# Kernel tuning notes

Measured on AMD Instinct MI355X. Metric: run time of the kernel, lower is better.

Reference implementation:

```python
import jax, jax.numpy as jnp
import numpy as np

N, D, H = 262144, 512, 128


def _mlp(x, W1, b1, W2, b2):
    # Linear -> ReLU -> Linear
    return jax.nn.relu(x @ W1 + b1) @ W2 + b2


def setup_inputs() -> dict:
    key = jax.random.key(0)
    ks = jax.random.split(key, 8)
    features = jax.random.normal(ks[0], (N, D), dtype=jnp.float32)
    # last column is the routing flag: 0 -> transform expert, nonzero -> actor expert
    flags = jax.random.randint(ks[1], (N,), 0, 2).astype(jnp.float32)
    features = features.at[:, -1].set(flags)
    s = 0.02
    return {
        "features": features,
        "Wt1": jax.random.normal(ks[2], (D, H), dtype=jnp.float32) * s,
        "bt1": jnp.zeros((H,), dtype=jnp.float32),
        "Wt2": jax.random.normal(ks[3], (H, H), dtype=jnp.float32) * s,
        "bt2": jnp.zeros((H,), dtype=jnp.float32),
        "Wa1": jax.random.normal(ks[4], (D, H), dtype=jnp.float32) * s,
        "ba1": jnp.zeros((H,), dtype=jnp.float32),
        "Wa2": jax.random.normal(ks[5], (H, H), dtype=jnp.float32) * s,
        "ba2": jnp.zeros((H,), dtype=jnp.float32),
        "Wv1": jax.random.normal(ks[6], (D, H), dtype=jnp.float32) * s,
        "bv1": jnp.zeros((H,), dtype=jnp.float32),
        "Wv2": jax.random.normal(ks[7], (H, H), dtype=jnp.float32) * s,
        "bv2": jnp.zeros((H,), dtype=jnp.float32),
    }


def reference(features, Wt1, bt1, Wt2, bt2, Wa1, ba1, Wa2, ba2, Wv1, bv1, Wv2, bv2):
    # forward_actor: per-row dispatch on flag = features[:, -1]
    # flag == 0 -> policy_transform_net, else -> policy_actor_net.
    # Equivalent vectorized form: compute both experts, select per row.
    flag_is_zero = (features[:, -1] == 0)[:, None]  # [N, 1]
    trans_out = _mlp(features, Wt1, bt1, Wt2, bt2)   # [N, H]
    actor_out = _mlp(features, Wa1, ba1, Wa2, ba2)   # [N, H]
    latent_pi = jnp.where(flag_is_zero, trans_out, actor_out)
    # forward_critic: Linear-ReLU-Linear-ReLU
    latent_vf = jax.nn.relu(_mlp(features, Wv1, bv1, Wv2, bv2))
    return latent_pi, latent_vf
```

## Files before the change

kernel.cpp:

```cpp
#include <hip/hip_runtime.h>

#define NTOK 262144L

typedef __attribute__((ext_vector_type(4))) float f32x4;
typedef __attribute__((ext_vector_type(8))) short bf16x8;

static __device__ __forceinline__ unsigned short f2bf(float f) {
  unsigned int u = __builtin_bit_cast(unsigned int, f);
  u += 0x7fffu + ((u >> 16) & 1u);
  return (unsigned short)(u >> 16);
}

__global__ void pack_w(const float* __restrict__ Wt1, const float* __restrict__ Wa1,
                       const float* __restrict__ Wv1, const float* __restrict__ Wt2,
                       const float* __restrict__ Wa2, const float* __restrict__ Wv2,
                       unsigned short* __restrict__ pk) {
  int idx = blockIdx.x * 256 + threadIdx.x;
  if (idx >= 245760) return;
  float v;
  if (idx < 196608) {
    int j = idx & 7, l = (idx >> 3) & 63, ct = (idx >> 9) & 7, kt = (idx >> 12) & 15, e = idx >> 16;
    const float* W = (e == 0) ? Wt1 : (e == 1) ? Wa1 : Wv1;
    v = W[(kt * 32 + ((l >> 4) * 8) + j) * 128 + ct * 16 + (l & 15)];
  } else {
    int i2 = idx - 196608;
    int j = i2 & 7, l = (i2 >> 3) & 63, ct = (i2 >> 9) & 7, kt = (i2 >> 12) & 3, e = i2 >> 14;
    const float* W = (e == 0) ? Wt2 : (e == 1) ? Wa2 : Wv2;
    v = W[(kt * 32 + ((l >> 4) * 8) + j) * 128 + ct * 16 + (l & 15)];
  }
  pk[idx] = f2bf(v);
}


__global__ __launch_bounds__(256, 4) void mlp3(
    const float* __restrict__ X, const unsigned short* __restrict__ pk,
    const float* __restrict__ bt1, const float* __restrict__ bt2,
    const float* __restrict__ ba1, const float* __restrict__ ba2,
    const float* __restrict__ bv1, const float* __restrict__ bv2,
    float* __restrict__ out) {
  __shared__ unsigned short Xs[2 * 32 * 128];
  __shared__ unsigned short H0[32 * 128];
  __shared__ unsigned short H1[32 * 128];
  const int t = threadIdx.x;
  const long brow = (long)blockIdx.x * 32;
  const int lane = t & 63;
  const int w = t >> 6;
  const int l15 = lane & 15;
  const int g = lane >> 4;

  const float4* __restrict__ Xv = (const float4*)(X + brow * 512);

  f32x4 at[2][2], aa[2][2], av[2][2];
  #pragma unroll
  for (int c = 0; c < 2; ++c) {
    float b0 = bt1[(2 * w + c) * 16 + l15];
    float b1v = ba1[(2 * w + c) * 16 + l15];
    float b2v = bv1[(2 * w + c) * 16 + l15];
    #pragma unroll
    for (int rt = 0; rt < 2; ++rt) {
      at[rt][c] = (f32x4){b0, b0, b0, b0};
      aa[rt][c] = (f32x4){b1v, b1v, b1v, b1v};
      av[rt][c] = (f32x4){b2v, b2v, b2v, b2v};
    }
  }

  {
    float4 ld[4];
    #pragma unroll
    for (int i = 0; i < 4; ++i) {
      int f = t + 256 * i;
      ld[i] = Xv[(f >> 5) * 128 + (f & 31)];
    }
    #pragma unroll
    for (int i = 0; i < 4; ++i) {
      int f = t + 256 * i;
      int row = f >> 5, c4 = f & 31;
      unsigned long long p = (unsigned long long)f2bf(ld[i].x)
                           | ((unsigned long long)f2bf(ld[i].y) << 16)
                           | ((unsigned long long)f2bf(ld[i].z) << 32)
                           | ((unsigned long long)f2bf(ld[i].w) << 48);
      int addr = (row * 256 + c4 * 8) ^ ((row & 7) << 4);
      *(unsigned long long*)((char*)Xs + addr) = p;
    }
  }
  __syncthreads();

  unsigned fmask = 0;

  #pragma unroll
  for (int kc = 0; kc < 4; ++kc) {
    float4 nx[4];
    if (kc < 3) {
      #pragma unroll
      for (int i = 0; i < 4; ++i) {
        int f = t + 256 * i;
        nx[i] = Xv[(f >> 5) * 128 + (kc + 1) * 32 + (f & 31)];
      }
    }
    const char* xb = (const char*)Xs + (kc & 1) * 8192;
    #pragma unroll
    for (int ktl = 0; ktl < 4; ++ktl) {
      int kt = kc * 4 + ktl;
      int wo0 = ((kt * 8 + 2 * w) << 9) + (lane << 3);
      bf16x8 wt0 = *(const bf16x8*)(pk + wo0);
      bf16x8 wt1v = *(const bf16x8*)(pk + wo0 + 512);
      bf16x8 wa0 = *(const bf16x8*)(pk + 65536 + wo0);
      bf16x8 wa1v = *(const bf16x8*)(pk + 65536 + wo0 + 512);
      bf16x8 wv0 = *(const bf16x8*)(pk + 131072 + wo0);
      bf16x8 wv1v = *(const bf16x8*)(pk + 131072 + wo0 + 512);
      #pragma unroll
      for (int rt = 0; rt < 2; ++rt) {
        int row = rt * 16 + l15;
        bf16x8 a = *(const bf16x8*)(xb + ((row * 256 + ktl * 64 + g * 16) ^ ((row & 7) << 4)));
        at[rt][0] = __builtin_amdgcn_mfma_f32_16x16x32_bf16(a, wt0, at[rt][0], 0, 0, 0);
        at[rt][1] = __builtin_amdgcn_mfma_f32_16x16x32_bf16(a, wt1v, at[rt][1], 0, 0, 0);
        aa[rt][0] = __builtin_amdgcn_mfma_f32_16x16x32_bf16(a, wa0, aa[rt][0], 0, 0, 0);
        aa[rt][1] = __builtin_amdgcn_mfma_f32_16x16x32_bf16(a, wa1v, aa[rt][1], 0, 0, 0);
        av[rt][0] = __builtin_amdgcn_mfma_f32_16x16x32_bf16(a, wv0, av[rt][0], 0, 0, 0);
        av[rt][1] = __builtin_amdgcn_mfma_f32_16x16x32_bf16(a, wv1v, av[rt][1], 0, 0, 0);
      }
    }
    if (kc == 3) {
      #pragma unroll
      for (int rt = 0; rt < 2; ++rt)
        #pragma unroll
        for (int r = 0; r < 4; ++r) {
          int row = rt * 16 + 4 * g + r;
          unsigned short fv = *(const unsigned short*)((const char*)Xs + 8192 +
                               ((row * 256 + 254) ^ ((row & 7) << 4)));
          if (fv != 0) fmask |= 1u << (rt * 4 + r);
        }
    }
    if (kc < 3) {
      #pragma unroll
      for (int i = 0; i < 4; ++i) {
        int f = t + 256 * i;
        int row = f >> 5, c4 = f & 31;
        unsigned long long p = (unsigned long long)f2bf(nx[i].x)
                             | ((unsigned long long)f2bf(nx[i].y) << 16)
                             | ((unsigned long long)f2bf(nx[i].z) << 32)
                             | ((unsigned long long)f2bf(nx[i].w) << 48);
        int addr = (((kc + 1) & 1) * 8192) + ((row * 256 + c4 * 8) ^ ((row & 7) << 4));
        *(unsigned long long*)((char*)Xs + addr) = p;
      }
      __syncthreads();
    }
  }

  #pragma unroll
  for (int rt = 0; rt < 2; ++rt)
    #pragma unroll
    for (int c = 0; c < 2; ++c)
      #pragma unroll
      for (int r = 0; r < 4; ++r) {
        int row = rt * 16 + 4 * g + r;
        int col = (2 * w + c) * 16 + l15;
        int ha = (row * 256 + col * 2) ^ ((row & 7) << 4) ^ ((row & 8) << 2);
        *(unsigned short*)((char*)H0 + ha) = f2bf(fmaxf(at[rt][c][r], 0.f));
        *(unsigned short*)((char*)H1 + ha) = f2bf(fmaxf(aa[rt][c][r], 0.f));
      }
  __syncthreads();

  auto layer2 = [&](const unsigned short* Hb, int e, const float* __restrict__ b2, f32x4 a2[2][2]) {
    #pragma unroll
    for (int c = 0; c < 2; ++c) {
      float bv = b2[(2 * w + c) * 16 + l15];
      a2[0][c] = (f32x4){bv, bv, bv, bv};
      a2[1][c] = (f32x4){bv, bv, bv, bv};
    }
    const unsigned short* W2f = pk + 196608 + e * 16384;
    #pragma unroll
    for (int kt = 0; kt < 4; ++kt) {
      int wo = ((kt * 8 + 2 * w) << 9) + (lane << 3);
      bf16x8 w0 = *(const bf16x8*)(W2f + wo);
      bf16x8 w1 = *(const bf16x8*)(W2f + wo + 512);
      #pragma unroll
      for (int rt = 0; rt < 2; ++rt) {
        int row = rt * 16 + l15;
        bf16x8 a = *(const bf16x8*)((const char*)Hb +
                     ((row * 256 + kt * 64 + g * 16) ^ ((row & 7) << 4) ^ ((row & 8) << 2)));
        a2[rt][0] = __builtin_amdgcn_mfma_f32_16x16x32_bf16(a, w0, a2[rt][0], 0, 0, 0);
        a2[rt][1] = __builtin_amdgcn_mfma_f32_16x16x32_bf16(a, w1, a2[rt][1], 0, 0, 0);
      }
    }
  };

  f32x4 keep[2][2], a2[2][2];
  layer2(H0, 0, bt2, keep);
  layer2(H1, 1, ba2, a2);
  #pragma unroll
  for (int rt = 0; rt < 2; ++rt)
    #pragma unroll
    for (int c = 0; c < 2; ++c)
      #pragma unroll
      for (int r = 0; r < 4; ++r)
        if ((fmask >> (rt * 4 + r)) & 1u) keep[rt][c][r] = a2[rt][c][r];
  __syncthreads();

  #pragma unroll
  for (int rt = 0; rt < 2; ++rt)
    #pragma unroll
    for (int c = 0; c < 2; ++c)
      #pragma unroll
      for (int r = 0; r < 4; ++r) {
        int row = rt * 16 + 4 * g + r;
        int col = (2 * w + c) * 16 + l15;
        int ha = (row * 256 + col * 2) ^ ((row & 7) << 4) ^ ((row & 8) << 2);
        *(unsigned short*)((char*)H0 + ha) = f2bf(fmaxf(av[rt][c][r], 0.f));
      }
  __syncthreads();
  layer2(H0, 2, bv2, a2);

  float* __restrict__ ov = out + NTOK * 128;
  #pragma unroll
  for (int rt = 0; rt < 2; ++rt)
    #pragma unroll
    for (int c = 0; c < 2; ++c)
      #pragma unroll
      for (int r = 0; r < 4; ++r) {
        long row = brow + rt * 16 + 4 * g + r;
        long col = (2 * w + c) * 16 + l15;
        out[row * 128 + col] = keep[rt][c][r];
        ov[row * 128 + col] = fmaxf(a2[rt][c][r], 0.f);
      }
}

extern "C" void kernel_launch(void* const* d_in, const int* in_sizes, int n_in,
                              void* d_out, int out_size, void* d_ws, size_t ws_size,
                              hipStream_t stream) {
  const float* X   = (const float*)d_in[0];
  const float* Wt1 = (const float*)d_in[1];
  const float* bt1 = (const float*)d_in[2];
  const float* Wt2 = (const float*)d_in[3];
  const float* bt2 = (const float*)d_in[4];
  const float* Wa1 = (const float*)d_in[5];
  const float* ba1 = (const float*)d_in[6];
  const float* Wa2 = (const float*)d_in[7];
  const float* ba2 = (const float*)d_in[8];
  const float* Wv1 = (const float*)d_in[9];
  const float* bv1 = (const float*)d_in[10];
  const float* Wv2 = (const float*)d_in[11];
  const float* bv2 = (const float*)d_in[12];
  unsigned short* pk = (unsigned short*)d_ws;

  pack_w<<<960, 256, 0, stream>>>(Wt1, Wa1, Wv1, Wt2, Wa2, Wv2, pk);
  mlp3<<<8192, 256, 0, stream>>>(X, pk, bt1, bt2, ba1, ba2, bv1, bv2, (float*)d_out);
}
```

Baseline: 271.9 us.

## Stream X via global_load_lds DMA as fp32 and convert to bf16 at MFMA load

Replaces the register-staged load/convert/store of X tiles with direct global-to-LDS DMA (global_load_lds) of fp32 data, using a new XOR swizzle. Conversion to bf16 now happens when A fragments are read from LDS, via v_cvt_pk_bf16_f32. The hidden-activation stores also use packed conversion, and s_setprio is raised around the MFMA loops. This removes VGPR staging and the per-element rounding ALU work from the load path, but doubles LDS usage for X and repeats the conversion for every A fragment read.

```diff
diff --git a/kernel.cpp b/kernel.cpp
--- a/kernel.cpp
+++ b/kernel.cpp
@@ -9,6 +9,27 @@
   unsigned int u = __builtin_bit_cast(unsigned int, f);
   u += 0x7fffu + ((u >> 16) & 1u);
   return (unsigned short)(u >> 16);
+}
+
+static __device__ __forceinline__ unsigned cvtpk(float lo, float hi) {
+  unsigned r;
+  asm("v_cvt_pk_bf16_f32 %0, %1, %2" : "=v"(r) : "v"(lo), "v"(hi));
+  return r;
+}
+
+union U8 { unsigned u[4]; bf16x8 v; };
+
+static __device__ __forceinline__ void dma16(const float* gsrc, void* ldst) {
+  __builtin_amdgcn_global_load_lds(
+      (const __attribute__((address_space(1))) unsigned int*)gsrc,
+      (__attribute__((address_space(3))) unsigned int*)ldst, 16, 0, 0);
+}
+
+static __device__ __forceinline__ int sigx(int row) {
+  return (row & 1) | ((row & 8) >> 2) | ((row & 6) << 2);
+}
+static __device__ __forceinline__ int swzh(int row) {
+  return ((row & 8) << 1) | ((row & 6) << 5);
 }
 
 __global__ void pack_w(const float* __restrict__ Wt1, const float* __restrict__ Wa1,
@@ -31,6 +52,34 @@
   pk[idx] = f2bf(v);
 }
 
+static __device__ __forceinline__ bf16x8 ldA(const char* xb, int row, int ktl, int g) {
+  int swz = sigx(row) << 4;
+  int base = row * 512 + ktl * 128 + g * 32;
+  f32x4 f0 = *(const f32x4*)(xb + (base ^ swz));
+  f32x4 f1 = *(const f32x4*)(xb + ((base + 16) ^ swz));
+  U8 r;
+  r.u[0] = cvtpk(f0[0], f0[1]);
+  r.u[1] = cvtpk(f0[2], f0[3]);
+  r.u[2] = cvtpk(f1[0], f1[1]);
+  r.u[3] = cvtpk(f1[2], f1[3]);
+  return r.v;
+}
+
+static __device__ __forceinline__ void stH(char* Hb, int g, int col, int rbase, f32x4 a) {
+  #pragma unroll
+  for (int rp = 0; rp < 2; ++rp) {
+    int r0 = rbase + 4 * g + 2 * rp;
+    unsigned p = cvtpk(fmaxf(a[2 * rp], 0.f), fmaxf(a[2 * rp + 1], 0.f));
+    int a0 = r0 * 256 + ((((col >> 3) << 4)) ^ swzh(r0)) + (col & 7) * 2;
+    int a1 = (r0 + 1) * 256 + ((((col >> 3) << 4)) ^ swzh(r0 + 1)) + (col & 7) * 2;
+    *(unsigned short*)(Hb + a0) = (unsigned short)p;
+    *(unsigned short*)(Hb + a1) = (unsigned short)(p >> 16);
+  }
+}
+
+static __device__ __forceinline__ bf16x8 ldH(const char* hb, int row, int kt, int g) {
+  return *(const bf16x8*)(hb + row * 256 + ((((kt * 4 + g) << 4)) ^ swzh(row)));
+}
 
 __global__ __launch_bounds__(256, 4) void mlp3(
     const float* __restrict__ X, const unsigned short* __restrict__ pk,
@@ -38,7 +87,7 @@
     const float* __restrict__ ba1, const float* __restrict__ ba2,
     const float* __restrict__ bv1, const float* __restrict__ bv2,
     float* __restrict__ out) {
-  __shared__ unsigned short Xs[2 * 32 * 128];
+  __shared__ float Xs[2 * 32 * 128];
   __shared__ unsigned short H0[32 * 128];
   __shared__ unsigned short H1[32 * 128];
   const int t = threadIdx.x;
@@ -48,7 +97,7 @@
   const int l15 = lane & 15;
   const int g = lane >> 4;
 
-  const float4* __restrict__ Xv = (const float4*)(X + brow * 512);
+  const float* __restrict__ Xrow = X + brow * 512;
 
   f32x4 at[2][2], aa[2][2], av[2][2];
   #pragma unroll
@@ -64,24 +113,12 @@
     }
   }
 
-  {
-    float4 ld[4];
-    #pragma unroll
-    for (int i = 0; i < 4; ++i) {
-      int f = t + 256 * i;
-      ld[i] = Xv[(f >> 5) * 128 + (f & 31)];
-    }
-    #pragma unroll
-    for (int i = 0; i < 4; ++i) {
-      int f = t + 256 * i;
-      int row = f >> 5, c4 = f & 31;
-      unsigned long long p = (unsigned long long)f2bf(ld[i].x)
-                           | ((unsigned long long)f2bf(ld[i].y) << 16)
-                           | ((unsigned long long)f2bf(ld[i].z) << 32)
-                           | ((unsigned long long)f2bf(ld[i].w) << 48);
-      int addr = (row * 256 + c4 * 8) ^ ((row & 7) << 4);
-      *(unsigned long long*)((char*)Xs + addr) = p;
-    }
+  #pragma unroll
+  for (int i = 0; i < 4; ++i) {
+    int lin = i * 256 + t;
+    int row = lin >> 5, S = lin & 31;
+    dma16(Xrow + row * 512 + ((S ^ sigx(row)) << 2),
+          (char*)Xs + i * 4096 + w * 1024);
   }
   __syncthreads();
 
@@ -89,15 +126,17 @@
 
   #pragma unroll
   for (int kc = 0; kc < 4; ++kc) {
-    float4 nx[4];
     if (kc < 3) {
       #pragma unroll
       for (int i = 0; i < 4; ++i) {
-        int f = t + 256 * i;
-        nx[i] = Xv[(f >> 5) * 128 + (kc + 1) * 32 + (f & 31)];
-      }
-    }
-    const char* xb = (const char*)Xs + (kc & 1) * 8192;
+        int lin = i * 256 + t;
+        int row = lin >> 5, S = lin & 31;
+        dma16(Xrow + row * 512 + (kc + 1) * 128 + ((S ^ sigx(row)) << 2),
+              (char*)Xs + ((kc + 1) & 1) * 16384 + i * 4096 + w * 1024);
+      }
+    }
+    const char* xb = (const char*)Xs + (kc & 1) * 16384;
+    __builtin_amdgcn_s_setprio(1);
     #pragma unroll
     for (int ktl = 0; ktl < 4; ++ktl) {
       int kt = kc * 4 + ktl;
@@ -110,8 +149,7 @@
       bf16x8 wv1v = *(const bf16x8*)(pk + 131072 + wo0 + 512);
       #pragma unroll
       for (int rt = 0; rt < 2; ++rt) {
-        int row = rt * 16 + l15;
-        bf16x8 a = *(const bf16x8*)(xb + ((row * 256 + ktl * 64 + g * 16) ^ ((row & 7) << 4)));
+        bf16x8 a = ldA(xb, rt * 16 + l15, ktl, g);
         at[rt][0] = __builtin_amdgcn_mfma_f32_16x16x32_bf16(a, wt0, at[rt][0], 0, 0, 0);
         at[rt][1] = __builtin_amdgcn_mfma_f32_16x16x32_bf16(a, wt1v, at[rt][1], 0, 0, 0);
         aa[rt][0] = __builtin_amdgcn_mfma_f32_16x16x32_bf16(a, wa0, aa[rt][0], 0, 0, 0);
@@ -120,45 +158,28 @@
         av[rt][1] = __builtin_amdgcn_mfma_f32_16x16x32_bf16(a, wv1v, av[rt][1], 0, 0, 0);
       }
     }
+    __builtin_amdgcn_s_setprio(0);
     if (kc == 3) {
       #pragma unroll
       for (int rt = 0; rt < 2; ++rt)
         #pragma unroll
         for (int r = 0; r < 4; ++r) {
           int row = rt * 16 + 4 * g + r;
-          unsigned short fv = *(const unsigned short*)((const char*)Xs + 8192 +
-                               ((row * 256 + 254) ^ ((row & 7) << 4)));
-          if (fv != 0) fmask |= 1u << (rt * 4 + r);
+          float fv = *(const float*)(xb + row * 512 + (((31 ^ sigx(row)) << 4)) + 12);
+          if (fv != 0.f) fmask |= 1u << (rt * 4 + r);
         }
     }
-    if (kc < 3) {
-      #pragma unroll
-      for (int i = 0; i < 4; ++i) {
-        int f = t + 256 * i;
-        int row = f >> 5, c4 = f & 31;
-        unsigned long long p = (unsigned long long)f2bf(nx[i].x)
-                             | ((unsigned long long)f2bf(nx[i].y) << 16)
-                             | ((unsigned long long)f2bf(nx[i].z) << 32)
-                             | ((unsigned long long)f2bf(nx[i].w) << 48);
-        int addr = (((kc + 1) & 1) * 8192) + ((row * 256 + c4 * 8) ^ ((row & 7) << 4));
-        *(unsigned long long*)((char*)Xs + addr) = p;
-      }
-      __syncthreads();
-    }
-  }
-
-  #pragma unroll
-  for (int rt = 0; rt < 2; ++rt)
-    #pragma unroll
-    for (int c = 0; c < 2; ++c)
-      #pragma unroll
-      for (int r = 0; r < 4; ++r) {
-        int row = rt * 16 + 4 * g + r;
-        int col = (2 * w + c) * 16 + l15;
-        int ha = (row * 256 + col * 2) ^ ((row & 7) << 4) ^ ((row & 8) << 2);
-        *(unsigned short*)((char*)H0 + ha) = f2bf(fmaxf(at[rt][c][r], 0.f));
-        *(unsigned short*)((char*)H1 + ha) = f2bf(fmaxf(aa[rt][c][r], 0.f));
-      }
+    if (kc < 3) __syncthreads();
+  }
+
+  #pragma unroll
+  for (int rt = 0; rt < 2; ++rt)
+    #pragma unroll
+    for (int c = 0; c < 2; ++c) {
+      int col = (2 * w + c) * 16 + l15;
+      stH((char*)H0, g, col, rt * 16, at[rt][c]);
+      stH((char*)H1, g, col, rt * 16, aa[rt][c]);
+    }
   __syncthreads();
 
   auto layer2 = [&](const unsigned short* Hb, int e, const float* __restrict__ b2, f32x4 a2[2][2]) {
@@ -169,6 +190,7 @@
       a2[1][c] = (f32x4){bv, bv, bv, bv};
     }
     const unsigned short* W2f = pk + 196608 + e * 16384;
+    __builtin_amdgcn_s_setprio(1);
     #pragma unroll
     for (int kt = 0; kt < 4; ++kt) {
       int wo = ((kt * 8 + 2 * w) << 9) + (lane << 3);
@@ -176,13 +198,12 @@
       bf16x8 w1 = *(const bf16x8*)(W2f + wo + 512);
       #pragma unroll
       for (int rt = 0; rt < 2; ++rt) {
-        int row = rt * 16 + l15;
-        bf16x8 a = *(const bf16x8*)((const char*)Hb +
-                     ((row * 256 + kt * 64 + g * 16) ^ ((row & 7) << 4) ^ ((row & 8) << 2)));
+        bf16x8 a = ldH((const char*)Hb, rt * 16 + l15, kt, g);
         a2[rt][0] = __builtin_amdgcn_mfma_f32_16x16x32_bf16(a, w0, a2[rt][0], 0, 0, 0);
         a2[rt][1] = __builtin_amdgcn_mfma_f32_16x16x32_bf16(a, w1, a2[rt][1], 0, 0, 0);
       }
     }
+    __builtin_amdgcn_s_setprio(0);
   };
 
   f32x4 keep[2][2], a2[2][2];
@@ -200,14 +221,10 @@
   #pragma unroll
   for (int rt = 0; rt < 2; ++rt)
     #pragma unroll
-    for (int c = 0; c < 2; ++c)
-      #pragma unroll
-      for (int r = 0; r < 4; ++r) {
-        int row = rt * 16 + 4 * g + r;
-        int col = (2 * w + c) * 16 + l15;
-        int ha = (row * 256 + col * 2) ^ ((row & 7) << 4) ^ ((row & 8) << 2);
-        *(unsigned short*)((char*)H0 + ha) = f2bf(fmaxf(av[rt][c][r], 0.f));
-      }
+    for (int c = 0; c < 2; ++c) {
+      int col = (2 * w + c) * 16 + l15;
+      stH((char*)H0, g, col, rt * 16, av[rt][c]);
+    }
   __syncthreads();
   layer2(H0, 2, bv2, a2);
 
```

Result: faster. 264.2 us (-2.8%).

## Double row tile to 64 per block with 64-wide K staging and packed bf16 converts

Applied to the files above, without the earlier changes.

Each block now handles 64 rows instead of 32, so every weight fragment loaded from global memory feeds twice as many MFMAs, halving weight traffic per row. X is staged in 64-column chunks, with each thread loading a contiguous 64-byte segment. The fp32-to-bf16 conversion uses the v_cvt_pk_bf16_f32 instruction, and the LDS swizzles are rewritten to match. s_setprio is raised around the MFMA loops. In exchange, register pressure rises (launch bounds drop to 3 blocks per CU), there are more syncs per K step, and the grid is half as large.

```diff
diff --git a/kernel.cpp b/kernel.cpp
--- a/kernel.cpp
+++ b/kernel.cpp
@@ -4,11 +4,18 @@
 
 typedef __attribute__((ext_vector_type(4))) float f32x4;
 typedef __attribute__((ext_vector_type(8))) short bf16x8;
+typedef __attribute__((ext_vector_type(4))) unsigned u32x4;
 
 static __device__ __forceinline__ unsigned short f2bf(float f) {
   unsigned int u = __builtin_bit_cast(unsigned int, f);
   u += 0x7fffu + ((u >> 16) & 1u);
   return (unsigned short)(u >> 16);
+}
+
+static __device__ __forceinline__ unsigned cvtpk(float lo, float hi) {
+  unsigned r;
+  asm("v_cvt_pk_bf16_f32 %0, %1, %2" : "=v"(r) : "v"(lo), "v"(hi));
+  return r;
 }
 
 __global__ void pack_w(const float* __restrict__ Wt1, const float* __restrict__ Wa1,
@@ -32,32 +39,37 @@
 }
 
 
-__global__ __launch_bounds__(256, 4) void mlp3(
+__global__ __launch_bounds__(256, 3) void mlp3(
     const float* __restrict__ X, const unsigned short* __restrict__ pk,
     const float* __restrict__ bt1, const float* __restrict__ bt2,
     const float* __restrict__ ba1, const float* __restrict__ ba2,
     const float* __restrict__ bv1, const float* __restrict__ bv2,
     float* __restrict__ out) {
-  __shared__ unsigned short Xs[2 * 32 * 128];
-  __shared__ unsigned short H0[32 * 128];
-  __shared__ unsigned short H1[32 * 128];
+  __shared__ unsigned short Xs[2 * 64 * 64];
+  __shared__ unsigned short H0[64 * 128];
+  __shared__ unsigned short H1[64 * 128];
   const int t = threadIdx.x;
-  const long brow = (long)blockIdx.x * 32;
+  const long brow = (long)blockIdx.x * 64;
   const int lane = t & 63;
   const int w = t >> 6;
   const int l15 = lane & 15;
   const int g = lane >> 4;
-
-  const float4* __restrict__ Xv = (const float4*)(X + brow * 512);
-
-  f32x4 at[2][2], aa[2][2], av[2][2];
+  char* const xs = (char*)Xs;
+
+  const int srow = t >> 2;
+  const int sseg = t & 3;
+  const float* __restrict__ sgp = X + (brow + srow) * 512 + sseg * 16;
+  const int wbyte0 = srow * 128 + ((((2 * sseg)) ^ (srow & 7)) << 4);
+  const int wbyte1 = srow * 128 + ((((2 * sseg + 1)) ^ (srow & 7)) << 4);
+
+  f32x4 at[4][2], aa[4][2], av[4][2];
   #pragma unroll
   for (int c = 0; c < 2; ++c) {
     float b0 = bt1[(2 * w + c) * 16 + l15];
     float b1v = ba1[(2 * w + c) * 16 + l15];
     float b2v = bv1[(2 * w + c) * 16 + l15];
     #pragma unroll
-    for (int rt = 0; rt < 2; ++rt) {
+    for (int rt = 0; rt < 4; ++rt) {
       at[rt][c] = (f32x4){b0, b0, b0, b0};
       aa[rt][c] = (f32x4){b1v, b1v, b1v, b1v};
       av[rt][c] = (f32x4){b2v, b2v, b2v, b2v};
@@ -65,53 +77,50 @@
   }
 
   {
-    float4 ld[4];
-    #pragma unroll
-    for (int i = 0; i < 4; ++i) {
-      int f = t + 256 * i;
-      ld[i] = Xv[(f >> 5) * 128 + (f & 31)];
-    }
-    #pragma unroll
-    for (int i = 0; i < 4; ++i) {
-      int f = t + 256 * i;
-      int row = f >> 5, c4 = f & 31;
-      unsigned long long p = (unsigned long long)f2bf(ld[i].x)
-                           | ((unsigned long long)f2bf(ld[i].y) << 16)
-                           | ((unsigned long long)f2bf(ld[i].z) << 32)
-                           | ((unsigned long long)f2bf(ld[i].w) << 48);
-      int addr = (row * 256 + c4 * 8) ^ ((row & 7) << 4);
-      *(unsigned long long*)((char*)Xs + addr) = p;
-    }
+    f32x4 q0 = *(const f32x4*)(sgp + 0);
+    f32x4 q1 = *(const f32x4*)(sgp + 4);
+    f32x4 q2 = *(const f32x4*)(sgp + 8);
+    f32x4 q3 = *(const f32x4*)(sgp + 12);
+    u32x4 p0 = {cvtpk(q0[0], q0[1]), cvtpk(q0[2], q0[3]), cvtpk(q1[0], q1[1]), cvtpk(q1[2], q1[3])};
+    u32x4 p1 = {cvtpk(q2[0], q2[1]), cvtpk(q2[2], q2[3]), cvtpk(q3[0], q3[1]), cvtpk(q3[2], q3[3])};
+    *(u32x4*)(xs + wbyte0) = p0;
+    *(u32x4*)(xs + wbyte1) = p1;
   }
   __syncthreads();
 
   unsigned fmask = 0;
 
-  #pragma unroll
-  for (int kc = 0; kc < 4; ++kc) {
-    float4 nx[4];
-    if (kc < 3) {
-      #pragma unroll
-      for (int i = 0; i < 4; ++i) {
-        int f = t + 256 * i;
-        nx[i] = Xv[(f >> 5) * 128 + (kc + 1) * 32 + (f & 31)];
-      }
-    }
-    const char* xb = (const char*)Xs + (kc & 1) * 8192;
-    #pragma unroll
-    for (int ktl = 0; ktl < 4; ++ktl) {
-      int kt = kc * 4 + ktl;
-      int wo0 = ((kt * 8 + 2 * w) << 9) + (lane << 3);
-      bf16x8 wt0 = *(const bf16x8*)(pk + wo0);
-      bf16x8 wt1v = *(const bf16x8*)(pk + wo0 + 512);
-      bf16x8 wa0 = *(const bf16x8*)(pk + 65536 + wo0);
-      bf16x8 wa1v = *(const bf16x8*)(pk + 65536 + wo0 + 512);
-      bf16x8 wv0 = *(const bf16x8*)(pk + 131072 + wo0);
-      bf16x8 wv1v = *(const bf16x8*)(pk + 131072 + wo0 + 512);
-      #pragma unroll
-      for (int rt = 0; rt < 2; ++rt) {
-        int row = rt * 16 + l15;
-        bf16x8 a = *(const bf16x8*)(xb + ((row * 256 + ktl * 64 + g * 16) ^ ((row & 7) << 4)));
+  const int abase = l15 * 128;
+  const int sx0 = ((0 * 4 + g) ^ (l15 & 7)) << 4;
+  const int sx1 = ((1 * 4 + g) ^ (l15 & 7)) << 4;
+
+  #pragma unroll 2
+  for (int kc = 0; kc < 8; ++kc) {
+    const bool st = kc < 7;
+    f32x4 q0, q1, q2, q3;
+    if (st) {
+      const float* gp = sgp + (kc + 1) * 64;
+      q0 = *(const f32x4*)(gp + 0);
+      q1 = *(const f32x4*)(gp + 4);
+      q2 = *(const f32x4*)(gp + 8);
+      q3 = *(const f32x4*)(gp + 12);
+    }
+    const char* xb = xs + ((kc & 1) << 13);
+    __builtin_amdgcn_s_setprio(1);
+    #pragma unroll
+    for (int ktl = 0; ktl < 2; ++ktl) {
+      const int kt = kc * 2 + ktl;
+      const int wo = ((kt * 8 + 2 * w) << 9) + (lane << 3);
+      bf16x8 wt0 = *(const bf16x8*)(pk + wo);
+      bf16x8 wt1v = *(const bf16x8*)(pk + wo + 512);
+      bf16x8 wa0 = *(const bf16x8*)(pk + 65536 + wo);
+      bf16x8 wa1v = *(const bf16x8*)(pk + 65536 + wo + 512);
+      bf16x8 wv0 = *(const bf16x8*)(pk + 131072 + wo);
+      bf16x8 wv1v = *(const bf16x8*)(pk + 131072 + wo + 512);
+      const int sx = ktl ? sx1 : sx0;
+      #pragma unroll
+      for (int rt = 0; rt < 4; ++rt) {
+        bf16x8 a = *(const bf16x8*)(xb + abase + rt * 2048 + sx);
         at[rt][0] = __builtin_amdgcn_mfma_f32_16x16x32_bf16(a, wt0, at[rt][0], 0, 0, 0);
         at[rt][1] = __builtin_amdgcn_mfma_f32_16x16x32_bf16(a, wt1v, at[rt][1], 0, 0, 0);
         aa[rt][0] = __builtin_amdgcn_mfma_f32_16x16x32_bf16(a, wa0, aa[rt][0], 0, 0, 0);
@@ -120,76 +129,74 @@
         av[rt][1] = __builtin_amdgcn_mfma_f32_16x16x32_bf16(a, wv1v, av[rt][1], 0, 0, 0);
       }
     }
-    if (kc == 3) {
-      #pragma unroll
-      for (int rt = 0; rt < 2; ++rt)
+    __builtin_amdgcn_s_setprio(0);
+    if (kc == 7) {
+      #pragma unroll
+      for (int rt = 0; rt < 4; ++rt)
         #pragma unroll
         for (int r = 0; r < 4; ++r) {
           int row = rt * 16 + 4 * g + r;
-          unsigned short fv = *(const unsigned short*)((const char*)Xs + 8192 +
-                               ((row * 256 + 254) ^ ((row & 7) << 4)));
+          unsigned short fv = *(const unsigned short*)(xs + 8192 + row * 128 +
+                               ((7 ^ (row & 7)) << 4) + 14);
           if (fv != 0) fmask |= 1u << (rt * 4 + r);
         }
     }
-    if (kc < 3) {
-      #pragma unroll
-      for (int i = 0; i < 4; ++i) {
-        int f = t + 256 * i;
-        int row = f >> 5, c4 = f & 31;
-        unsigned long long p = (unsigned long long)f2bf(nx[i].x)
-                             | ((unsigned long long)f2bf(nx[i].y) << 16)
-                             | ((unsigned long long)f2bf(nx[i].z) << 32)
-                             | ((unsigned long long)f2bf(nx[i].w) << 48);
-        int addr = (((kc + 1) & 1) * 8192) + ((row * 256 + c4 * 8) ^ ((row & 7) << 4));
-        *(unsigned long long*)((char*)Xs + addr) = p;
-      }
-      __syncthreads();
-    }
-  }
-
-  #pragma unroll
-  for (int rt = 0; rt < 2; ++rt)
+    if (st) {
+      char* xw = xs + (((kc + 1) & 1) << 13);
+      u32x4 p0 = {cvtpk(q0[0], q0[1]), cvtpk(q0[2], q0[3]), cvtpk(q1[0], q1[1]), cvtpk(q1[2], q1[3])};
+      u32x4 p1 = {cvtpk(q2[0], q2[1]), cvtpk(q2[2], q2[3]), cvtpk(q3[0], q3[1]), cvtpk(q3[2], q3[3])};
+      *(u32x4*)(xw + wbyte0) = p0;
+      *(u32x4*)(xw + wbyte1) = p1;
+    }
+    __syncthreads();
+  }
+
+  #pragma unroll
+  for (int rt = 0; rt < 4; ++rt)
     #pragma unroll
     for (int c = 0; c < 2; ++c)
       #pragma unroll
       for (int r = 0; r < 4; ++r) {
         int row = rt * 16 + 4 * g + r;
-        int col = (2 * w + c) * 16 + l15;
-        int ha = (row * 256 + col * 2) ^ ((row & 7) << 4) ^ ((row & 8) << 2);
-        *(unsigned short*)((char*)H0 + ha) = f2bf(fmaxf(at[rt][c][r], 0.f));
-        *(unsigned short*)((char*)H1 + ha) = f2bf(fmaxf(aa[rt][c][r], 0.f));
-      }
-  __syncthreads();
-
-  auto layer2 = [&](const unsigned short* Hb, int e, const float* __restrict__ b2, f32x4 a2[2][2]) {
+        int slot = (4 * w + 2 * c + (l15 >> 3)) ^ (row & 7);
+        int addr = row * 256 + (slot << 4) + (l15 & 7) * 2;
+        *(unsigned short*)((char*)H0 + addr) = f2bf(fmaxf(at[rt][c][r], 0.f));
+        *(unsigned short*)((char*)H1 + addr) = f2bf(fmaxf(aa[rt][c][r], 0.f));
+      }
+  __syncthreads();
+
+  const int hbase = l15 * 256;
+  auto layer2 = [&](const unsigned short* Hb, int e, const float* __restrict__ b2,
+                    f32x4 a2[4][2]) {
     #pragma unroll
     for (int c = 0; c < 2; ++c) {
       float bv = b2[(2 * w + c) * 16 + l15];
-      a2[0][c] = (f32x4){bv, bv, bv, bv};
-      a2[1][c] = (f32x4){bv, bv, bv, bv};
+      #pragma unroll
+      for (int rt = 0; rt < 4; ++rt) a2[rt][c] = (f32x4){bv, bv, bv, bv};
     }
     const unsigned short* W2f = pk + 196608 + e * 16384;
+    __builtin_amdgcn_s_setprio(1);
     #pragma unroll
     for (int kt = 0; kt < 4; ++kt) {
-      int wo = ((kt * 8 + 2 * w) << 9) + (lane << 3);
+      const int wo = ((kt * 8 + 2 * w) << 9) + (lane << 3);
       bf16x8 w0 = *(const bf16x8*)(W2f + wo);
       bf16x8 w1 = *(const bf16x8*)(W2f + wo + 512);
-      #pragma unroll
-      for (int rt = 0; rt < 2; ++rt) {
-        int row = rt * 16 + l15;
-        bf16x8 a = *(const bf16x8*)((const char*)Hb +
-                     ((row * 256 + kt * 64 + g * 16) ^ ((row & 7) << 4) ^ ((row & 8) << 2)));
+      const int hs = ((kt * 4 + g) ^ (l15 & 7)) << 4;
+      #pragma unroll
+      for (int rt = 0; rt < 4; ++rt) {
+        bf16x8 a = *(const bf16x8*)((const char*)Hb + hbase + rt * 4096 + hs);
         a2[rt][0] = __builtin_amdgcn_mfma_f32_16x16x32_bf16(a, w0, a2[rt][0], 0, 0, 0);
         a2[rt][1] = __builtin_amdgcn_mfma_f32_16x16x32_bf16(a, w1, a2[rt][1], 0, 0, 0);
       }
     }
+    __builtin_amdgcn_s_setprio(0);
   };
 
-  f32x4 keep[2][2], a2[2][2];
+  f32x4 keep[4][2], a2[4][2];
   layer2(H0, 0, bt2, keep);
   layer2(H1, 1, ba2, a2);
   #pragma unroll
-  for (int rt = 0; rt < 2; ++rt)
+  for (int rt = 0; rt < 4; ++rt)
     #pragma unroll
     for (int c = 0; c < 2; ++c)
       #pragma unroll
@@ -198,22 +205,22 @@
   __syncthreads();
 
   #pragma unroll
-  for (int rt = 0; rt < 2; ++rt)
+  for (int rt = 0; rt < 4; ++rt)
     #pragma unroll
     for (int c = 0; c < 2; ++c)
       #pragma unroll
       for (int r = 0; r < 4; ++r) {
         int row = rt * 16 + 4 * g + r;
-        int col = (2 * w + c) * 16 + l15;
-        int ha = (row * 256 + col * 2) ^ ((row & 7) << 4) ^ ((row & 8) << 2);
-        *(unsigned short*)((char*)H0 + ha) = f2bf(fmaxf(av[rt][c][r], 0.f));
+        int slot = (4 * w + 2 * c + (l15 >> 3)) ^ (row & 7);
+        int addr = row * 256 + (slot << 4) + (l15 & 7) * 2;
+        *(unsigned short*)((char*)H0 + addr) = f2bf(fmaxf(av[rt][c][r], 0.f));
       }
   __syncthreads();
   layer2(H0, 2, bv2, a2);
 
   float* __restrict__ ov = out + NTOK * 128;
   #pragma unroll
-  for (int rt = 0; rt < 2; ++rt)
+  for (int rt = 0; rt < 4; ++rt)
     #pragma unroll
     for (int c = 0; c < 2; ++c)
       #pragma unroll
@@ -244,5 +251,5 @@
   unsigned short* pk = (unsigned short*)d_ws;
 
   pack_w<<<960, 256, 0, stream>>>(Wt1, Wa1, Wv1, Wt2, Wa2, Wv2, pk);
-  mlp3<<<8192, 256, 0, stream>>>(X, pk, bt1, bt2, ba1, ba2, bv1, bv2, (float*)d_out);
-}
+  mlp3<<<4096, 256, 0, stream>>>(X, pk, bt1, bt2, ba1, ba2, bv1, bv2, (float*)d_out);
+}
```

Result: slower. 371.9 us (+36.8%).
